# Kernel optimization log

Hardware: AMD Instinct MI355X
Metric: run time of the kernel (lower is better)

The kernel has to match this reference:

```python
import jax, jax.numpy as jnp
import numpy as np

EPS = 1e-7  # K.epsilon()
N_ROUTINGS = 3


def squash(v, axis=-1):
    s2 = jnp.sum(jnp.square(v), axis=axis, keepdims=True)
    scale = s2 / (1.0 + s2) / jnp.sqrt(s2 + EPS)
    return scale * v


def setup_inputs() -> dict:
    key = jax.random.key(0)
    k1, k2 = jax.random.split(key)
    B, IN_CAPS, IN_DIM = 128, 1152, 8
    N_CAPS, DIM = 32, 16
    inputs = jax.random.normal(k1, (B, IN_CAPS, IN_DIM), dtype=jnp.float32)
    # glorot-uniform-ish scale for W [n_capsule, in_caps, dim_capsule, in_dim]
    limit = np.sqrt(6.0 / (IN_DIM + DIM)).astype(np.float32)
    W = jax.random.uniform(k2, (N_CAPS, IN_CAPS, DIM, IN_DIM), dtype=jnp.float32,
                           minval=-limit, maxval=limit)
    return {"inputs": inputs, "W": W}


def reference(inputs, W):
    # inputs: [b, i, l]; W: [j, i, k, l] -> u_hat: [b, j, i, k]
    u_hat = jnp.einsum('jikl,bil->bjik', W, inputs)
    b = jnp.zeros(u_hat.shape[:3], dtype=u_hat.dtype)  # [b, j, i]
    v = None
    for r in range(N_ROUTINGS):
        c = jax.nn.softmax(b, axis=1)                 # softmax over output caps j
        s = jnp.einsum('bji,bjik->bjk', c, u_hat)     # weighted sum over input caps i
        v = squash(s, axis=-1)                        # [b, j, k]
        if r < N_ROUTINGS - 1:
            b = b + jnp.einsum('bjik,bjk->bji', u_hat, v)  # agreement
    return v
```

## Files before the change

kernel.cpp:

```cpp
#include <hip/hip_runtime.h>
#include <hip/hip_bf16.h>
#include <stdint.h>


using fab = __attribute__((ext_vector_type(8))) short;
using fcc = __attribute__((ext_vector_type(4))) float;

__device__ __forceinline__ uint32_t bfr(float f) {
    uint32_t u = __float_as_uint(f);
    return (u + 0x7fffu + ((u >> 16) & 1u)) >> 16;
}

__global__ __launch_bounds__(256)
void prep(const float* __restrict__ W, const float* __restrict__ x,
          ushort* __restrict__ W3, ushort* __restrict__ X2)
{
    const int t = blockIdx.x * 256 + threadIdx.x;
    {
        const int k = t & 15, j = (t >> 4) & 31, i = t >> 9;
        const float* src = W + (((size_t)j * 1152 + i) * 16 + k) * 8;
        const float4 a = *reinterpret_cast<const float4*>(src);
        const float4 b = *reinterpret_cast<const float4*>(src + 4);
        uint4 o;
        o.x = bfr(a.x) | (bfr(a.y) << 16);
        o.y = bfr(a.z) | (bfr(a.w) << 16);
        o.z = bfr(b.x) | (bfr(b.y) << 16);
        o.w = bfr(b.z) | (bfr(b.w) << 16);
        *reinterpret_cast<uint4*>(W3 + (size_t)t * 8) = o;
    }
    if (t < 147456) {
        const int b = t & 127, i = t >> 7;
        const float* src = x + ((size_t)b * 1152 + i) * 8;
        const float4 a = *reinterpret_cast<const float4*>(src);
        const float4 bb = *reinterpret_cast<const float4*>(src + 4);
        uint4 o;
        o.x = bfr(a.x) | (bfr(a.y) << 16);
        o.y = bfr(a.z) | (bfr(a.w) << 16);
        o.z = bfr(bb.x) | (bfr(bb.y) << 16);
        o.w = bfr(bb.z) | (bfr(bb.w) << 16);
        *reinterpret_cast<uint4*>(X2 + (size_t)t * 8) = o;
    }
}

__global__ __launch_bounds__(512)
void caps_route0(const ushort* __restrict__ W3,
                 const ushort* __restrict__ X2,
                 float* __restrict__ sout)
{
    __shared__ float tr[8][1024];

    const int tid  = threadIdx.x;
    const int lane = tid & 63;
    const int w    = tid >> 6;
    const int bl   = lane & 15;
    const int kg   = lane >> 4;
    const int bg   = blockIdx.x >> 6;
    const int sl   = blockIdx.x & 63;
    const int i0   = sl * 18;
    const int b0   = bg * 16;

    fab zf;
    #pragma unroll
    for (int q = 0; q < 8; ++q) zf[q] = 0;

    auto loadAq = [&](int g, int t, bool ok) -> fab {
        return ok ? *reinterpret_cast<const fab*>(
                       W3 + (((size_t)(i0 + 4 * g + kg) * 32 + w * 4 + t) * 16 + bl) * 8)
                  : zf;
    };
    auto loadBq = [&](int g, bool ok) -> fab {
        return ok ? *reinterpret_cast<const fab*>(
                       X2 + ((size_t)(i0 + 4 * g + kg) * 128 + b0 + bl) * 8)
                  : zf;
    };

    fcc sacc[4];
    #pragma unroll
    for (int t = 0; t < 4; ++t)
        #pragma unroll
        for (int r = 0; r < 4; ++r) sacc[t][r] = 0.0f;

    fab Ac[4], An[4], Bc, Bn;
    #pragma unroll
    for (int t = 0; t < 4; ++t) Ac[t] = loadAq(0, t, true);
    Bc = loadBq(0, true);

    #pragma unroll
    for (int g = 0; g < 5; ++g) {
        if (g < 4) {
            const bool ok = (g + 1 < 4) | (kg < 2);
            #pragma unroll
            for (int t = 0; t < 4; ++t) An[t] = loadAq(g + 1, t, ok);
            Bn = loadBq(g + 1, ok);
        }
        #pragma unroll
        for (int t = 0; t < 4; ++t)
            sacc[t] = __builtin_amdgcn_mfma_f32_16x16x32_bf16(Ac[t], Bc, sacc[t], 0, 0, 0);
        if (g < 4) {
            #pragma unroll
            for (int t = 0; t < 4; ++t) Ac[t] = An[t];
            Bc = Bn;
        }
    }

    {
        float* ep = &tr[w][0];
        #pragma unroll
        for (int t = 0; t < 4; ++t)
            #pragma unroll
            for (int r = 0; r < 4; ++r) {
                const int off = t * 16 + kg * 4 + r;
                ep[off * 16 + (bl ^ (off & 15))] = sacc[t][r] * 0.03125f;
            }
        float* sg = sout + (size_t)b0 * 512 + w * 64;
        #pragma unroll
        for (int c = 0; c < 16; ++c) {
            const float v = ep[lane * 16 + (c ^ (lane & 15))];
            atomicAdd(&sg[(size_t)c * 512 + lane], v);
        }
    }
}

template<int R>
__global__ __launch_bounds__(512, 4)
void caps_route_sm(const ushort* __restrict__ W3,
                   const ushort* __restrict__ X2,
                   const float* __restrict__ s0,
                   const float* __restrict__ s1,
                   float* __restrict__ sout)
{
    __shared__ float pl[2][8][16][2];
    __shared__ float tr[8][1024];

    const int tid  = threadIdx.x;
    const int lane = tid & 63;
    const int w    = tid >> 6;
    const int bl   = lane & 15;
    const int kg   = lane >> 4;
    const bool lo  = (kg == 0);
    const int bg   = blockIdx.x >> 6;
    const int sl   = blockIdx.x & 63;
    const int i0   = sl * 18;
    const int b0   = bg * 16;

    fab zf;
    #pragma unroll
    for (int q = 0; q < 8; ++q) zf[q] = 0;

    auto loadA = [&](int i, int t) -> fab {
        return lo ? *reinterpret_cast<const fab*>(
                        W3 + (((size_t)i * 32 + w * 4 + t) * 16 + bl) * 8)
                  : zf;
    };
    auto loadB = [&](int i) -> fab {
        return lo ? *reinterpret_cast<const fab*>(
                        X2 + ((size_t)i * 128 + b0 + bl) * 8)
                  : zf;
    };

    float Vr[4][4];
    #pragma unroll
    for (int t = 0; t < 4; ++t) {
        const size_t ro = ((size_t)(b0 + bl) * 32 + w * 4 + t) * 16 + kg * 4;
        const float4 a = *reinterpret_cast<const float4*>(s0 + ro);
        float q = a.x * a.x + a.y * a.y + a.z * a.z + a.w * a.w;
        q += __shfl_xor(q, 16);
        q += __shfl_xor(q, 32);
        const float sc = q / ((1.0f + q) * sqrtf(q + 1e-7f)) * 1.44269504f;
        Vr[t][0] = a.x * sc; Vr[t][1] = a.y * sc;
        Vr[t][2] = a.z * sc; Vr[t][3] = a.w * sc;
        if (R == 2) {
            const float4 b = *reinterpret_cast<const float4*>(s1 + ro);
            float q1 = b.x * b.x + b.y * b.y + b.z * b.z + b.w * b.w;
            q1 += __shfl_xor(q1, 16);
            q1 += __shfl_xor(q1, 32);
            const float sc1 = q1 / ((1.0f + q1) * sqrtf(q1 + 1e-7f)) * 1.44269504f;
            Vr[t][0] += b.x * sc1; Vr[t][1] += b.y * sc1;
            Vr[t][2] += b.z * sc1; Vr[t][3] += b.w * sc1;
        }
    }

    fcc sacc[4];
    #pragma unroll
    for (int t = 0; t < 4; ++t)
        #pragma unroll
        for (int r = 0; r < 4; ++r) sacc[t][r] = 0.0f;

    const fcc cz = {0.0f, 0.0f, 0.0f, 0.0f};

    fab A0[4], A1[4], B0, B1;
    #pragma unroll
    for (int t = 0; t < 4; ++t) A0[t] = loadA(i0, t);
    B0 = loadB(i0);

    for (int pp = 0; pp < 9; ++pp) {
        const int ie = i0 + 2 * pp;
        #pragma unroll
        for (int t = 0; t < 4; ++t) A1[t] = loadA(ie + 1, t);
        B1 = loadB(ie + 1);

        fcc ue[4];
        #pragma unroll
        for (int t = 0; t < 4; ++t)
            ue[t] = __builtin_amdgcn_mfma_f32_16x16x32_bf16(A0[t], B0, cz, 0, 0, 0);
        float ee[4], pse = 0.0f;
        #pragma unroll
        for (int t = 0; t < 4; ++t) {
            float p = ue[t][0] * Vr[t][0];
            p = fmaf(ue[t][1], Vr[t][1], p);
            p = fmaf(ue[t][2], Vr[t][2], p);
            p = fmaf(ue[t][3], Vr[t][3], p);
            p += __shfl_xor(p, 16);
            p += __shfl_xor(p, 32);
            ee[t] = exp2f(p);
            pse += ee[t];
        }
        if (lane < 16) pl[pp & 1][w][bl][0] = pse;

        if (pp < 8) {
            #pragma unroll
            for (int t = 0; t < 4; ++t) A0[t] = loadA(ie + 2, t);
            B0 = loadB(ie + 2);
        }

        fcc uo[4];
        #pragma unroll
        for (int t = 0; t < 4; ++t)
            uo[t] = __builtin_amdgcn_mfma_f32_16x16x32_bf16(A1[t], B1, cz, 0, 0, 0);
        float eo[4], pso = 0.0f;
        #pragma unroll
        for (int t = 0; t < 4; ++t) {
            float p = uo[t][0] * Vr[t][0];
            p = fmaf(uo[t][1], Vr[t][1], p);
            p = fmaf(uo[t][2], Vr[t][2], p);
            p = fmaf(uo[t][3], Vr[t][3], p);
            p += __shfl_xor(p, 16);
            p += __shfl_xor(p, 32);
            eo[t] = exp2f(p);
            pso += eo[t];
        }
        if (lane >= 16 && lane < 32) pl[pp & 1][w][bl][1] = pso;

        __syncthreads();

        float dene = 0.0f, deno = 0.0f;
        #pragma unroll
        for (int ww = 0; ww < 8; ++ww) {
            const float2 d = *reinterpret_cast<const float2*>(&pl[pp & 1][ww][bl][0]);
            dene += d.x;
            deno += d.y;
        }
        const float inve = __builtin_amdgcn_rcpf(dene);
        const float invo = __builtin_amdgcn_rcpf(deno);
        #pragma unroll
        for (int t = 0; t < 4; ++t) {
            const float cfe = ee[t] * inve;
            const float cfo = eo[t] * invo;
            #pragma unroll
            for (int r = 0; r < 4; ++r) {
                sacc[t][r] = fmaf(cfe, ue[t][r], sacc[t][r]);
                sacc[t][r] = fmaf(cfo, uo[t][r], sacc[t][r]);
            }
        }
    }

    {
        float* ep = &tr[w][0];
        #pragma unroll
        for (int t = 0; t < 4; ++t)
            #pragma unroll
            for (int r = 0; r < 4; ++r) {
                const int off = t * 16 + kg * 4 + r;
                ep[off * 16 + (bl ^ (off & 15))] = sacc[t][r];
            }
        float* sg = sout + (size_t)b0 * 512 + w * 64;
        #pragma unroll
        for (int c = 0; c < 16; ++c) {
            const float v = ep[lane * 16 + (c ^ (lane & 15))];
            atomicAdd(&sg[(size_t)c * 512 + lane], v);
        }
    }
}

__global__ __launch_bounds__(256)
void caps_squash_out(const float* __restrict__ s2, float* __restrict__ out)
{
    const int t = blockIdx.x * 256 + threadIdx.x;
    const float sv = s2[t];
    float p = sv * sv;
    p += __shfl_xor(p, 1);
    p += __shfl_xor(p, 2);
    p += __shfl_xor(p, 4);
    p += __shfl_xor(p, 8);
    const float scale = p / ((1.0f + p) * sqrtf(p + 1e-7f));
    out[t] = scale * sv;
}

#define WJ        (1152 * 128)
#define I_TILE_F  24
#define NSLICE_F  48

template<int R>
__global__ __launch_bounds__(256)
void caps_route_f32(const float* __restrict__ x,
                    const float* __restrict__ W,
                    const float* __restrict__ Vacc,
                    float* __restrict__ s)
{
    __shared__ float Wt[2][4096];
    __shared__ float xs[8 * 192];

    const int tid  = threadIdx.x;
    const int lane = tid & 63;
    const int wv   = tid >> 6;
    const int j    = lane & 31;
    const int kh   = lane >> 5;
    const int bg   = blockIdx.x / NSLICE_F;
    const int sl   = blockIdx.x % NSLICE_F;
    const int i0   = sl * I_TILE_F;
    const int b0   = bg * 8 + wv * 2;

    const float* wsrc[4];
    #pragma unroll
    for (int t = 0; t < 4; ++t) {
        const int q  = (wv * 4 + t) * 1024 + lane * 16;
        const int rr = q >> 8;
        const int cb = (q & 255) ^ ((rr & 15) << 4);
        const int js = rr & 31;
        const int c  = (rr >> 5) * 64 + (cb >> 2);
        wsrc[t] = W + (size_t)js * WJ + c;
    }

    auto stage = [&](int buf, int i) {
        #pragma unroll
        for (int t = 0; t < 4; ++t)
            __builtin_amdgcn_global_load_lds(
                (const __attribute__((address_space(1))) uint32_t*)
                    (wsrc[t] + (size_t)i * 128),
                (__attribute__((address_space(3))) uint32_t*)
                    &Wt[buf][(wv * 4 + t) * 256], 16, 0, 0);
    };

    stage(0, i0);

    for (int cf = tid; cf < 384; cf += 256) {
        const int bl = cf / 48;
        const int rm = cf - bl * 48;
        float4 v = *reinterpret_cast<const float4*>(
            x + ((size_t)(bg * 8 + bl) * 1152 + i0) * 8 + rm * 4);
        *reinterpret_cast<float4*>(xs + bl * 192 + rm * 4) = v;
    }

    float Vr[2][8];
    if (R > 0) {
        #pragma unroll
        for (int bb = 0; bb < 2; ++bb) {
            const float* vp = Vacc + ((size_t)(b0 + bb) * 32 + j) * 16 + kh * 8;
            const float4 va = *reinterpret_cast<const float4*>(vp);
            const float4 vb = *reinterpret_cast<const float4*>(vp + 4);
            Vr[bb][0] = va.x * 1.44269504f; Vr[bb][1] = va.y * 1.44269504f;
            Vr[bb][2] = va.z * 1.44269504f; Vr[bb][3] = va.w * 1.44269504f;
            Vr[bb][4] = vb.x * 1.44269504f; Vr[bb][5] = vb.y * 1.44269504f;
            Vr[bb][6] = vb.z * 1.44269504f; Vr[bb][7] = vb.w * 1.44269504f;
        }
    }

    float sacc[2][8];
    #pragma unroll
    for (int bb = 0; bb < 2; ++bb)
        #pragma unroll
        for (int kk = 0; kk < 8; ++kk) sacc[bb][kk] = 0.0f;

    __syncthreads();

    const int sw = (j & 15) << 4;

    for (int ii = 0; ii < I_TILE_F; ++ii) {
        const int cur = ii & 1;
        if (ii + 1 < I_TILE_F) stage(cur ^ 1, i0 + ii + 1);

        float4 xa[2], xb[2];
        #pragma unroll
        for (int bb = 0; bb < 2; ++bb) {
            const float* xp = xs + (wv * 2 + bb) * 192 + ii * 8;
            xa[bb] = *reinterpret_cast<const float4*>(xp);
            xb[bb] = *reinterpret_cast<const float4*>(xp + 4);
        }

        const char* lbase = reinterpret_cast<const char*>(&Wt[cur][0]) + lane * 256;

        float u[2][8];
        #pragma unroll
        for (int kk = 0; kk < 8; ++kk) {
            const float4 w0 = *reinterpret_cast<const float4*>(lbase + ((kk * 32) ^ sw));
            const float4 w1 = *reinterpret_cast<const float4*>(lbase + ((kk * 32 + 16) ^ sw));
            #pragma unroll
            for (int bb = 0; bb < 2; ++bb) {
                float acc;
                acc = w0.x * xa[bb].x;
                acc = fmaf(w0.y, xa[bb].y, acc);
                acc = fmaf(w0.z, xa[bb].z, acc);
                acc = fmaf(w0.w, xa[bb].w, acc);
                acc = fmaf(w1.x, xb[bb].x, acc);
                acc = fmaf(w1.y, xb[bb].y, acc);
                acc = fmaf(w1.z, xb[bb].z, acc);
                acc = fmaf(w1.w, xb[bb].w, acc);
                u[bb][kk] = acc;
            }
        }

        if (R == 0) {
            #pragma unroll
            for (int bb = 0; bb < 2; ++bb)
                #pragma unroll
                for (int kk = 0; kk < 8; ++kk)
                    sacc[bb][kk] = fmaf(0.03125f, u[bb][kk], sacc[bb][kk]);
        } else {
            float p0 = u[0][0] * Vr[0][0];
            float p1 = u[1][0] * Vr[1][0];
            #pragma unroll
            for (int kk = 1; kk < 8; ++kk) {
                p0 = fmaf(u[0][kk], Vr[0][kk], p0);
                p1 = fmaf(u[1][kk], Vr[1][kk], p1);
            }
            p0 += __shfl_xor(p0, 32);
            p1 += __shfl_xor(p1, 32);
            const float pq = kh ? p1 : p0;
            const float e  = exp2f(pq);
            float den = e;
            den += __shfl_xor(den, 1);
            den += __shfl_xor(den, 2);
            den += __shfl_xor(den, 4);
            den += __shfl_xor(den, 8);
            den += __shfl_xor(den, 16);
            const float cf_own = e * __builtin_amdgcn_rcpf(den);
            const float cf_oth = __shfl_xor(cf_own, 32);
            const float cf0 = kh ? cf_oth : cf_own;
            const float cf1 = kh ? cf_own : cf_oth;
            #pragma unroll
            for (int kk = 0; kk < 8; ++kk) {
                sacc[0][kk] = fmaf(cf0, u[0][kk], sacc[0][kk]);
                sacc[1][kk] = fmaf(cf1, u[1][kk], sacc[1][kk]);
            }
        }
        __syncthreads();
    }

    {
        float* ep = &Wt[0][0] + wv * 1024;
        #pragma unroll
        for (int bb = 0; bb < 2; ++bb)
            #pragma unroll
            for (int kk = 0; kk < 8; ++kk)
                ep[bb * 512 + j * 16 + ((kh * 8 + kk) ^ ((j >> 1) & 15))] =
                    sacc[bb][kk];

        float* sg = s + (size_t)b0 * 512;
        #pragma unroll
        for (int c = 0; c < 16; ++c) {
            const int m   = c * 64 + lane;
            const int bb2 = m >> 9;
            const int j2  = (m >> 4) & 31;
            const int k2  = m & 15;
            const float v = ep[bb2 * 512 + j2 * 16 + (k2 ^ ((j2 >> 1) & 15))];
            atomicAdd(&sg[m], v);
        }
    }
}

template<int MODE>
__global__ __launch_bounds__(256)
void caps_squash(float* __restrict__ s,
                 float* __restrict__ Vacc,
                 float* __restrict__ out)
{
    const int t = blockIdx.x * 256 + threadIdx.x;
    const float sv = s[t];
    float p = sv * sv;
    p += __shfl_xor(p, 1);
    p += __shfl_xor(p, 2);
    p += __shfl_xor(p, 4);
    p += __shfl_xor(p, 8);
    const float scale = p / ((1.0f + p) * sqrtf(p + 1e-7f));
    const float v = scale * sv;
    if (MODE == 0)      { Vacc[t] = v;  s[t] = 0.0f; }
    else if (MODE == 1) { Vacc[t] += v; s[t] = 0.0f; }
    else                { out[t] = v; }
}

extern "C" void kernel_launch(void* const* d_in, const int* in_sizes, int n_in,
                              void* d_out, int out_size, void* d_ws, size_t ws_size,
                              hipStream_t stream)
{
    const float* x = (const float*)d_in[0];
    const float* W = (const float*)d_in[1];
    float* out = (float*)d_out;

    const size_t W3B = (size_t)589824 * 16;
    const size_t X2B = (size_t)147456 * 16;
    const size_t SB  = (size_t)65536 * sizeof(float);

    if (ws_size >= W3B + X2B + 3 * SB) {
        ushort* W3 = (ushort*)d_ws;
        ushort* X2 = (ushort*)((char*)d_ws + W3B);
        float* s0  = (float*)((char*)d_ws + W3B + X2B);
        float* s1  = s0 + 65536;
        float* s2  = s1 + 65536;

        hipMemsetAsync(s0, 0, 3 * SB, stream);
        prep<<<2304, 256, 0, stream>>>(W, x, W3, X2);

        dim3 grid(512);
        dim3 blk(512);
        caps_route0<<<grid, blk, 0, stream>>>(W3, X2, s0);
        caps_route_sm<1><<<grid, blk, 0, stream>>>(W3, X2, s0, s0, s1);
        caps_route_sm<2><<<grid, blk, 0, stream>>>(W3, X2, s0, s1, s2);
        caps_squash_out<<<256, 256, 0, stream>>>(s2, out);
    } else {
        float* Vacc = (float*)d_ws;
        float* sbuf = Vacc + 65536;
        hipMemsetAsync(sbuf, 0, SB, stream);

        dim3 grid(16 * NSLICE_F);
        dim3 blk(256);
        caps_route_f32<0><<<grid, blk, 0, stream>>>(x, W, Vacc, sbuf);
        caps_squash<0><<<256, 256, 0, stream>>>(sbuf, Vacc, out);
        caps_route_f32<1><<<grid, blk, 0, stream>>>(x, W, Vacc, sbuf);
        caps_squash<1><<<256, 256, 0, stream>>>(sbuf, Vacc, out);
        caps_route_f32<2><<<grid, blk, 0, stream>>>(x, W, Vacc, sbuf);
        caps_squash<2><<<256, 256, 0, stream>>>(sbuf, Vacc, out);
    }
}
```

Before: 105.7 us.

## Switch routing kernels to 32x32x16 MFMA with 32-batch tiles

The two softmax-routing kernels now use the 32x32x16 bf16 MFMA instead of 16x16x32 and process 32 batch rows per block rather than 16, which halves their grid to 256 blocks. The agreement dot product now needs one cross-lane shuffle instead of two, and the two-step unrolled loop becomes a single-step prefetch loop. The goal is fewer MFMA and shuffle instructions and half as many wavefront-wide softmax reductions per input capsule. In exchange the blocks hold more registers and twice the shared-memory transpose buffer, the occupancy hint is dropped, and fewer blocks means less latency hiding.

```diff
diff --git a/kernel.cpp b/kernel.cpp
--- a/kernel.cpp
+++ b/kernel.cpp
@@ -3,8 +3,9 @@
 #include <stdint.h>
 
 
-using fab = __attribute__((ext_vector_type(8))) short;
-using fcc = __attribute__((ext_vector_type(4))) float;
+using fab  = __attribute__((ext_vector_type(8)))  short;
+using fcc  = __attribute__((ext_vector_type(4)))  float;
+using fc16 = __attribute__((ext_vector_type(16))) float;
 
 __device__ __forceinline__ uint32_t bfr(float f) {
     uint32_t u = __float_as_uint(f);
@@ -122,161 +123,147 @@
 }
 
 template<int R>
-__global__ __launch_bounds__(512, 4)
+__global__ __launch_bounds__(512)
 void caps_route_sm(const ushort* __restrict__ W3,
                    const ushort* __restrict__ X2,
                    const float* __restrict__ s0,
                    const float* __restrict__ s1,
                    float* __restrict__ sout)
 {
-    __shared__ float pl[2][8][16][2];
-    __shared__ float tr[8][1024];
+    __shared__ float pl[2][8][32];
+    __shared__ float tr[8][2048];
 
     const int tid  = threadIdx.x;
     const int lane = tid & 63;
     const int w    = tid >> 6;
-    const int bl   = lane & 15;
-    const int kg   = lane >> 4;
-    const bool lo  = (kg == 0);
+    const int bc   = lane & 31;
+    const int h    = lane >> 5;
+    const bool lo  = (h == 0);
     const int bg   = blockIdx.x >> 6;
     const int sl   = blockIdx.x & 63;
     const int i0   = sl * 18;
-    const int b0   = bg * 16;
+    const int b0   = bg * 32;
 
     fab zf;
     #pragma unroll
     for (int q = 0; q < 8; ++q) zf[q] = 0;
 
-    auto loadA = [&](int i, int t) -> fab {
+    auto loadA = [&](int i, int m) -> fab {
         return lo ? *reinterpret_cast<const fab*>(
-                        W3 + (((size_t)i * 32 + w * 4 + t) * 16 + bl) * 8)
+                        W3 + (((size_t)i * 32 + w * 4 + m * 2 + (bc >> 4)) * 16
+                              + (bc & 15)) * 8)
                   : zf;
     };
     auto loadB = [&](int i) -> fab {
         return lo ? *reinterpret_cast<const fab*>(
-                        X2 + ((size_t)i * 128 + b0 + bl) * 8)
+                        X2 + ((size_t)i * 128 + b0 + bc) * 8)
                   : zf;
     };
 
-    float Vr[4][4];
-    #pragma unroll
-    for (int t = 0; t < 4; ++t) {
-        const size_t ro = ((size_t)(b0 + bl) * 32 + w * 4 + t) * 16 + kg * 4;
-        const float4 a = *reinterpret_cast<const float4*>(s0 + ro);
-        float q = a.x * a.x + a.y * a.y + a.z * a.z + a.w * a.w;
-        q += __shfl_xor(q, 16);
+    float Vr[4][8];
+    #pragma unroll
+    for (int jj = 0; jj < 4; ++jj) {
+        const size_t ro = ((size_t)(b0 + bc) * 32 + w * 4 + jj) * 16;
+        const float4 a0 = *reinterpret_cast<const float4*>(s0 + ro + 4 * h);
+        const float4 a1 = *reinterpret_cast<const float4*>(s0 + ro + 8 + 4 * h);
+        float q = a0.x * a0.x + a0.y * a0.y + a0.z * a0.z + a0.w * a0.w
+                + a1.x * a1.x + a1.y * a1.y + a1.z * a1.z + a1.w * a1.w;
         q += __shfl_xor(q, 32);
         const float sc = q / ((1.0f + q) * sqrtf(q + 1e-7f)) * 1.44269504f;
-        Vr[t][0] = a.x * sc; Vr[t][1] = a.y * sc;
-        Vr[t][2] = a.z * sc; Vr[t][3] = a.w * sc;
+        Vr[jj][0] = a0.x * sc; Vr[jj][1] = a0.y * sc;
+        Vr[jj][2] = a0.z * sc; Vr[jj][3] = a0.w * sc;
+        Vr[jj][4] = a1.x * sc; Vr[jj][5] = a1.y * sc;
+        Vr[jj][6] = a1.z * sc; Vr[jj][7] = a1.w * sc;
         if (R == 2) {
-            const float4 b = *reinterpret_cast<const float4*>(s1 + ro);
-            float q1 = b.x * b.x + b.y * b.y + b.z * b.z + b.w * b.w;
-            q1 += __shfl_xor(q1, 16);
+            const float4 b0v = *reinterpret_cast<const float4*>(s1 + ro + 4 * h);
+            const float4 b1v = *reinterpret_cast<const float4*>(s1 + ro + 8 + 4 * h);
+            float q1 = b0v.x * b0v.x + b0v.y * b0v.y + b0v.z * b0v.z + b0v.w * b0v.w
+                     + b1v.x * b1v.x + b1v.y * b1v.y + b1v.z * b1v.z + b1v.w * b1v.w;
             q1 += __shfl_xor(q1, 32);
             const float sc1 = q1 / ((1.0f + q1) * sqrtf(q1 + 1e-7f)) * 1.44269504f;
-            Vr[t][0] += b.x * sc1; Vr[t][1] += b.y * sc1;
-            Vr[t][2] += b.z * sc1; Vr[t][3] += b.w * sc1;
-        }
-    }
-
-    fcc sacc[4];
-    #pragma unroll
-    for (int t = 0; t < 4; ++t)
-        #pragma unroll
-        for (int r = 0; r < 4; ++r) sacc[t][r] = 0.0f;
-
-    const fcc cz = {0.0f, 0.0f, 0.0f, 0.0f};
-
-    fab A0[4], A1[4], B0, B1;
-    #pragma unroll
-    for (int t = 0; t < 4; ++t) A0[t] = loadA(i0, t);
-    B0 = loadB(i0);
-
-    for (int pp = 0; pp < 9; ++pp) {
-        const int ie = i0 + 2 * pp;
-        #pragma unroll
-        for (int t = 0; t < 4; ++t) A1[t] = loadA(ie + 1, t);
-        B1 = loadB(ie + 1);
-
-        fcc ue[4];
-        #pragma unroll
-        for (int t = 0; t < 4; ++t)
-            ue[t] = __builtin_amdgcn_mfma_f32_16x16x32_bf16(A0[t], B0, cz, 0, 0, 0);
-        float ee[4], pse = 0.0f;
-        #pragma unroll
-        for (int t = 0; t < 4; ++t) {
-            float p = ue[t][0] * Vr[t][0];
-            p = fmaf(ue[t][1], Vr[t][1], p);
-            p = fmaf(ue[t][2], Vr[t][2], p);
-            p = fmaf(ue[t][3], Vr[t][3], p);
-            p += __shfl_xor(p, 16);
-            p += __shfl_xor(p, 32);
-            ee[t] = exp2f(p);
-            pse += ee[t];
-        }
-        if (lane < 16) pl[pp & 1][w][bl][0] = pse;
-
-        if (pp < 8) {
-            #pragma unroll
-            for (int t = 0; t < 4; ++t) A0[t] = loadA(ie + 2, t);
-            B0 = loadB(ie + 2);
-        }
-
-        fcc uo[4];
-        #pragma unroll
-        for (int t = 0; t < 4; ++t)
-            uo[t] = __builtin_amdgcn_mfma_f32_16x16x32_bf16(A1[t], B1, cz, 0, 0, 0);
-        float eo[4], pso = 0.0f;
-        #pragma unroll
-        for (int t = 0; t < 4; ++t) {
-            float p = uo[t][0] * Vr[t][0];
-            p = fmaf(uo[t][1], Vr[t][1], p);
-            p = fmaf(uo[t][2], Vr[t][2], p);
-            p = fmaf(uo[t][3], Vr[t][3], p);
-            p += __shfl_xor(p, 16);
-            p += __shfl_xor(p, 32);
-            eo[t] = exp2f(p);
-            pso += eo[t];
-        }
-        if (lane >= 16 && lane < 32) pl[pp & 1][w][bl][1] = pso;
-
+            Vr[jj][0] += b0v.x * sc1; Vr[jj][1] += b0v.y * sc1;
+            Vr[jj][2] += b0v.z * sc1; Vr[jj][3] += b0v.w * sc1;
+            Vr[jj][4] += b1v.x * sc1; Vr[jj][5] += b1v.y * sc1;
+            Vr[jj][6] += b1v.z * sc1; Vr[jj][7] += b1v.w * sc1;
+        }
+    }
+
+    fc16 sacc[2];
+    #pragma unroll
+    for (int m = 0; m < 2; ++m)
+        #pragma unroll
+        for (int r = 0; r < 16; ++r) sacc[m][r] = 0.0f;
+
+    const fc16 cz16 = {0,0,0,0, 0,0,0,0, 0,0,0,0, 0,0,0,0};
+
+    fab Ac[2], An[2], Bc, Bn;
+    #pragma unroll
+    for (int m = 0; m < 2; ++m) Ac[m] = loadA(i0, m);
+    Bc = loadB(i0);
+
+    for (int ii = 0; ii < 18; ++ii) {
+        {
+            int ip = i0 + ii + 1;
+            if (ip > 1151) ip = 1151;
+            #pragma unroll
+            for (int m = 0; m < 2; ++m) An[m] = loadA(ip, m);
+            Bn = loadB(ip);
+        }
+
+        fc16 u[2];
+        #pragma unroll
+        for (int m = 0; m < 2; ++m)
+            u[m] = __builtin_amdgcn_mfma_f32_32x32x16_bf16(Ac[m], Bc, cz16, 0, 0, 0);
+
+        float e[4];
+        float esum = 0.0f;
+        #pragma unroll
+        for (int m = 0; m < 2; ++m)
+            #pragma unroll
+            for (int j2 = 0; j2 < 2; ++j2) {
+                const int jj = m * 2 + j2;
+                float p = u[m][j2 * 8 + 0] * Vr[jj][0];
+                #pragma unroll
+                for (int s = 1; s < 8; ++s)
+                    p = fmaf(u[m][j2 * 8 + s], Vr[jj][s], p);
+                p += __shfl_xor(p, 32);
+                e[jj] = exp2f(p);
+                esum += e[jj];
+            }
+
+        const int ib = ii & 1;
+        if (h == 0) pl[ib][w][bc] = esum;
         __syncthreads();
-
-        float dene = 0.0f, deno = 0.0f;
-        #pragma unroll
-        for (int ww = 0; ww < 8; ++ww) {
-            const float2 d = *reinterpret_cast<const float2*>(&pl[pp & 1][ww][bl][0]);
-            dene += d.x;
-            deno += d.y;
-        }
-        const float inve = __builtin_amdgcn_rcpf(dene);
-        const float invo = __builtin_amdgcn_rcpf(deno);
-        #pragma unroll
-        for (int t = 0; t < 4; ++t) {
-            const float cfe = ee[t] * inve;
-            const float cfo = eo[t] * invo;
-            #pragma unroll
-            for (int r = 0; r < 4; ++r) {
-                sacc[t][r] = fmaf(cfe, ue[t][r], sacc[t][r]);
-                sacc[t][r] = fmaf(cfo, uo[t][r], sacc[t][r]);
-            }
-        }
+        float den = pl[ib][0][bc];
+        #pragma unroll
+        for (int ww = 1; ww < 8; ++ww) den += pl[ib][ww][bc];
+        const float inv = __builtin_amdgcn_rcpf(den);
+
+        #pragma unroll
+        for (int m = 0; m < 2; ++m)
+            #pragma unroll
+            for (int r = 0; r < 16; ++r)
+                sacc[m][r] = fmaf(e[m * 2 + (r >> 3)] * inv, u[m][r], sacc[m][r]);
+
+        #pragma unroll
+        for (int m = 0; m < 2; ++m) Ac[m] = An[m];
+        Bc = Bn;
     }
 
     {
         float* ep = &tr[w][0];
         #pragma unroll
-        for (int t = 0; t < 4; ++t)
-            #pragma unroll
-            for (int r = 0; r < 4; ++r) {
-                const int off = t * 16 + kg * 4 + r;
-                ep[off * 16 + (bl ^ (off & 15))] = sacc[t][r];
+        for (int m = 0; m < 2; ++m)
+            #pragma unroll
+            for (int r = 0; r < 16; ++r) {
+                const int off = (m * 2 + (r >> 3)) * 16
+                              + (r & 3) + 8 * ((r >> 2) & 1) + 4 * h;
+                ep[off * 32 + (bc ^ (off & 31))] = sacc[m][r];
             }
         float* sg = sout + (size_t)b0 * 512 + w * 64;
         #pragma unroll
-        for (int c = 0; c < 16; ++c) {
-            const float v = ep[lane * 16 + (c ^ (lane & 15))];
+        for (int c = 0; c < 32; ++c) {
+            const float v = ep[lane * 32 + (c ^ (lane & 31))];
             atomicAdd(&sg[(size_t)c * 512 + lane], v);
         }
     }
@@ -510,11 +497,9 @@
         hipMemsetAsync(s0, 0, 3 * SB, stream);
         prep<<<2304, 256, 0, stream>>>(W, x, W3, X2);
 
-        dim3 grid(512);
-        dim3 blk(512);
-        caps_route0<<<grid, blk, 0, stream>>>(W3, X2, s0);
-        caps_route_sm<1><<<grid, blk, 0, stream>>>(W3, X2, s0, s0, s1);
-        caps_route_sm<2><<<grid, blk, 0, stream>>>(W3, X2, s0, s1, s2);
+        caps_route0<<<512, 512, 0, stream>>>(W3, X2, s0);
+        caps_route_sm<1><<<256, 512, 0, stream>>>(W3, X2, s0, s0, s1);
+        caps_route_sm<2><<<256, 512, 0, stream>>>(W3, X2, s0, s1, s2);
         caps_squash_out<<<256, 256, 0, stream>>>(s2, out);
     } else {
         float* Vacc = (float*)d_ws;
```

Measured after the change: 108.0 us. +2.2%, slower.
